# Kernel optimization log

Measured on AMD Instinct MI355X. Metric: run time of the kernel, lower is better.

## Reference

```python
import jax, jax.numpy as jnp
import numpy as np

EPS = 1e-8  # matches torch cosine_similarity eps


def setup_inputs() -> dict:
    key = jax.random.key(0)
    ks = jax.random.split(key, 8)
    B, D_IN, H, L = 256, 256, 256, 100000
    G = 5 * H  # (N_GATES + 1) * hidden_dim
    s_in = 1.0 / np.sqrt(D_IN)
    s_h = 1.0 / np.sqrt(H)
    return {
        "x_t": jax.random.normal(ks[0], (B, D_IN), jnp.float32),
        "h": jax.random.normal(ks[1], (B, H), jnp.float32),
        "c": jax.random.normal(ks[2], (B, H), jnp.float32),
        "W_i2h": jax.random.normal(ks[3], (G, D_IN), jnp.float32) * s_in,
        "b_i2h": jnp.zeros((G,), jnp.float32),
        "W_h2h": jax.random.normal(ks[4], (G, H), jnp.float32) * s_h,
        "b_h2h": jnp.zeros((G,), jnp.float32),
        "keys": jax.random.normal(ks[5], (L, D_IN), jnp.float32),
        "vals": jax.random.normal(ks[6], (L, H), jnp.float32),
    }


def _dnd_get_memory(q, keys, vals):
    # cosine similarity of each query against every stored key -> [B, L]
    qn = q / jnp.maximum(jnp.linalg.norm(q, axis=-1, keepdims=True), EPS)
    kn = keys / jnp.maximum(jnp.linalg.norm(keys, axis=-1, keepdims=True), EPS)
    sims = jnp.einsum("bd,ld->bl", qn, kn)
    w = jax.nn.softmax(sims, axis=-1)          # softmax-weighted aggregation
    return jnp.einsum("bl,lh->bh", w, vals)    # [B, H]


def reference(x_t, h, c, W_i2h, b_i2h, W_h2h, b_h2h, keys, vals):
    H = h.shape[1]
    preact = (x_t @ W_i2h.T + b_i2h) + (h @ W_h2h.T + b_h2h)   # [B, 5H]
    gates = jax.nn.sigmoid(preact[:, : 4 * H])
    f_t = gates[:, :H]
    i_t = gates[:, H:2 * H]
    o_t = gates[:, 2 * H:3 * H]
    r_t = gates[:, 3 * H:4 * H]
    c_t_new = jnp.tanh(preact[:, 4 * H:])
    c_t = f_t * c + i_t * c_t_new
    m_t = jnp.tanh(_dnd_get_memory(x_t, keys, vals))
    c_t = c_t + r_t * m_t
    h_t = o_t * jnp.tanh(c_t)
    return (h_t, c_t)
```

## Files before the change

### kernel.cpp

```cpp
#include <hip/hip_runtime.h>
#include <stdint.h>

typedef float f4_t __attribute__((ext_vector_type(4)));
typedef __bf16 bf8_t __attribute__((ext_vector_type(8)));
typedef unsigned short us4_t __attribute__((ext_vector_type(4)));
typedef unsigned short us8_t __attribute__((ext_vector_type(8)));

static __device__ __forceinline__ unsigned short fbf(float f) {
    __bf16 b = (__bf16)f;
    return *(unsigned short*)&b;
}
static __device__ __forceinline__ float bf2f(unsigned short u) {
    union { uint32_t u; float f; } v; v.u = ((uint32_t)u) << 16;
    return v.f;
}
static __device__ __forceinline__ f4_t mfma16(bf8_t a, bf8_t b, f4_t c) {
    return __builtin_amdgcn_mfma_f32_16x16x32_bf16(a, b, c, 0, 0, 0);
}
static __device__ __forceinline__ float sigf(float x) {
    return 1.0f / (1.0f + __expf(-x));
}
static __device__ __forceinline__ void gload_lds16(const void* g, void* l) {
    __builtin_amdgcn_global_load_lds(
        (const __attribute__((address_space(1))) void*)g,
        (__attribute__((address_space(3))) void*)l, 16, 0, 0);
}

__global__ __launch_bounds__(256) void k_convert(
    const float* __restrict__ x, const float* __restrict__ h,
    const float* __restrict__ W1, const float* __restrict__ W2,
    unsigned short* __restrict__ qn, unsigned short* __restrict__ xb,
    unsigned short* __restrict__ hb, unsigned short* __restrict__ w1b,
    unsigned short* __restrict__ w2b)
{
    __shared__ float sred[4];
    int bid = blockIdx.x, t = threadIdx.x;
    if (bid < 256) {
        float v = x[bid * 256 + t];
        float ss = v * v;
        #pragma unroll
        for (int m = 1; m < 64; m <<= 1) ss += __shfl_xor(ss, m, 64);
        if ((t & 63) == 0) sred[t >> 6] = ss;
        __syncthreads();
        float tot = sred[0] + sred[1] + sred[2] + sred[3];
        float rn = 1.0f / fmaxf(sqrtf(tot), 1e-8f);
        xb[bid * 256 + t] = fbf(v);
        qn[bid * 256 + t] = fbf(v * rn);
    } else if (bid < 512) {
        int b = bid - 256;
        hb[b * 256 + t] = fbf(h[b * 256 + t]);
    } else {
        int i0 = (bid - 512) * 256 + t;
        for (int i = i0; i < 1280 * 256; i += 512 * 256) {
            w1b[i] = fbf(W1[i]);
            w2b[i] = fbf(W2[i]);
        }
    }
}

__global__ __launch_bounds__(256) void k_gates(
    const unsigned short* __restrict__ xb, const unsigned short* __restrict__ hb,
    const unsigned short* __restrict__ w1b, const unsigned short* __restrict__ w2b,
    const float* __restrict__ b1, const float* __restrict__ b2,
    float* __restrict__ pre)
{
    int bb = (blockIdx.x & 3) * 64;
    int gb = (blockIdx.x >> 2) * 64;
    int t = threadIdx.x, w = t >> 6, lane = t & 63;
    int l15 = lane & 15, q8 = (lane >> 4) * 8, q4 = (lane >> 4) * 4;
    int arow = bb + w * 16 + l15;

    f4_t acc[4] = {};
    #pragma unroll
    for (int ks = 0; ks < 8; ++ks) {
        bf8_t a = *(const bf8_t*)&xb[arow * 256 + ks * 32 + q8];
        #pragma unroll
        for (int gc = 0; gc < 4; ++gc) {
            bf8_t bf = *(const bf8_t*)&w1b[(gb + gc * 16 + l15) * 256 + ks * 32 + q8];
            acc[gc] = mfma16(a, bf, acc[gc]);
        }
    }
    #pragma unroll
    for (int ks = 0; ks < 8; ++ks) {
        bf8_t a = *(const bf8_t*)&hb[arow * 256 + ks * 32 + q8];
        #pragma unroll
        for (int gc = 0; gc < 4; ++gc) {
            bf8_t bf = *(const bf8_t*)&w2b[(gb + gc * 16 + l15) * 256 + ks * 32 + q8];
            acc[gc] = mfma16(a, bf, acc[gc]);
        }
    }
    #pragma unroll
    for (int gc = 0; gc < 4; ++gc) {
        int g = gb + gc * 16 + l15;
        float bias = b1[g] + b2[g];
        #pragma unroll
        for (int r = 0; r < 4; ++r) {
            int b = bb + w * 16 + q4 + r;
            pre[b * 1280 + g] = acc[gc][r] + bias;
        }
    }
}

__global__ __launch_bounds__(512, 2) void k_dnd(
    const float* __restrict__ keys, const float* __restrict__ vals,
    const unsigned short* __restrict__ qn,
    unsigned short* __restrict__ opart, float* __restrict__ dpart,
    int L, int CH)
{
    __shared__ __align__(16) char smem[114688];
    unsigned short* Pl = (unsigned short*)(smem + 98304);

    const int t = threadIdx.x;
    const int w = t >> 6, lane = t & 63;
    const int l15 = lane & 15;
    const int q8 = (lane >> 4) * 8, q4 = (lane >> 4) * 4;

    const int bid = blockIdx.x;
    const int hhalf = (bid >> 3) & 1;
    const int chunk = (bid & 7) | ((bid >> 4) << 3);
    const int base = chunk * CH;
    int nkeys = L - base;
    if (nkeys > CH) nkeys = CH;
    if (nkeys < 0) nkeys = 0;
    const int nt = (nkeys + 31) >> 5;

    bf8_t qa[2][8];
    #pragma unroll
    for (int bt = 0; bt < 2; ++bt)
        #pragma unroll
        for (int ks = 0; ks < 8; ++ks)
            qa[bt][ks] = *(const bf8_t*)&qn[(w * 32 + bt * 16 + l15) * 256 + ks * 32 + q8];

    f4_t o[2][8] = {};
    float den[2][4] = {};

    auto issueRaw = [&](int tt) {
        #pragma unroll
        for (int i = 0; i < 4; ++i) {
            int lrow = 4 * w + i;
            int row = base + tt * 32 + lrow;
            if (row >= L) row = L - 1;
            gload_lds16(keys + (size_t)row * 256 + lane * 4,
                        smem + lrow * 1024);
        }
        #pragma unroll
        for (int c = 0; c < 2; ++c) {
            int lrow = 4 * w + 2 * c;
            int row = base + tt * 32 + lrow + (lane >> 5);
            if (row >= L) row = L - 1;
            gload_lds16(vals + (size_t)row * 256 + hhalf * 128 + (lane & 31) * 4,
                        smem + 32768 + lrow * 512);
        }
    };

    auto convert = [&](int buf) {
        unsigned short* Kb = (unsigned short*)(smem + 49152 + buf * 16384);
        unsigned short* Vb = (unsigned short*)(smem + 81920 + buf * 8192);
        const float* Kraw = (const float*)smem;
        const float* Vraw = (const float*)(smem + 32768);
        {
            int row = t >> 4, c16 = (t & 15) * 16;
            f4_t a0 = *(const f4_t*)&Kraw[row * 256 + c16];
            f4_t a1 = *(const f4_t*)&Kraw[row * 256 + c16 + 4];
            f4_t a2 = *(const f4_t*)&Kraw[row * 256 + c16 + 8];
            f4_t a3 = *(const f4_t*)&Kraw[row * 256 + c16 + 12];
            float ss = a0[0]*a0[0]+a0[1]*a0[1]+a0[2]*a0[2]+a0[3]*a0[3]
                     + a1[0]*a1[0]+a1[1]*a1[1]+a1[2]*a1[2]+a1[3]*a1[3]
                     + a2[0]*a2[0]+a2[1]*a2[1]+a2[2]*a2[2]+a2[3]*a2[3]
                     + a3[0]*a3[0]+a3[1]*a3[1]+a3[2]*a3[2]+a3[3]*a3[3];
            ss += __shfl_xor(ss, 1, 64);
            ss += __shfl_xor(ss, 2, 64);
            ss += __shfl_xor(ss, 4, 64);
            ss += __shfl_xor(ss, 8, 64);
            float rn = 1.0f / fmaxf(sqrtf(ss), 1e-8f);
            int sw = (row & 7) * 8;
            us8_t u0, u1;
            u0[0]=fbf(a0[0]*rn); u0[1]=fbf(a0[1]*rn); u0[2]=fbf(a0[2]*rn); u0[3]=fbf(a0[3]*rn);
            u0[4]=fbf(a1[0]*rn); u0[5]=fbf(a1[1]*rn); u0[6]=fbf(a1[2]*rn); u0[7]=fbf(a1[3]*rn);
            u1[0]=fbf(a2[0]*rn); u1[1]=fbf(a2[1]*rn); u1[2]=fbf(a2[2]*rn); u1[3]=fbf(a2[3]*rn);
            u1[4]=fbf(a3[0]*rn); u1[5]=fbf(a3[1]*rn); u1[6]=fbf(a3[2]*rn); u1[7]=fbf(a3[3]*rn);
            *(us8_t*)&Kb[row * 256 + (c16 ^ sw)]       = u0;
            *(us8_t*)&Kb[row * 256 + ((c16 + 8) ^ sw)] = u1;
        }
        {
            int hh = t & 127, oct = t >> 7;
            us8_t uv;
            #pragma unroll
            for (int r = 0; r < 8; ++r)
                uv[r] = fbf(Vraw[(oct * 8 + r) * 128 + hh]);
            int slot = (((hh & 15) * 4 + oct) ^ ((hh & 14) >> 1));
            *(us8_t*)&Vb[(hh >> 4) * 512 + slot * 8] = uv;
        }
    };

    if (nt > 0) {
        issueRaw(0);
        asm volatile("s_waitcnt vmcnt(0)" ::: "memory");
        __builtin_amdgcn_s_barrier();
        convert(0);
        asm volatile("s_waitcnt lgkmcnt(0)\n\ts_barrier" ::: "memory");
        if (nt > 1) issueRaw(1);

        for (int tt = 0; tt < nt; ++tt) {
            const int cur = tt & 1;
            const unsigned short* Kb = (const unsigned short*)(smem + 49152 + cur * 16384);
            const unsigned short* Vb = (const unsigned short*)(smem + 81920 + cur * 8192);

            f4_t s[2][2] = {};
            __builtin_amdgcn_s_setprio(1);
            #pragma unroll
            for (int lc = 0; lc < 2; ++lc) {
                int l = lc * 16 + l15;
                int sw = (l & 7) * 8;
                #pragma unroll
                for (int ks = 0; ks < 8; ++ks) {
                    bf8_t kf = *(const bf8_t*)&Kb[l * 256 + ((ks * 32 + q8) ^ sw)];
                    s[0][lc] = mfma16(qa[0][ks], kf, s[0][lc]);
                    s[1][lc] = mfma16(qa[1][ks], kf, s[1][lc]);
                }
            }
            __builtin_amdgcn_s_setprio(0);

            #pragma unroll
            for (int lc = 0; lc < 2; ++lc) {
                int l = lc * 16 + l15;
                bool valid = (tt * 32 + l) < nkeys;
                #pragma unroll
                for (int bt = 0; bt < 2; ++bt)
                    #pragma unroll
                    for (int r = 0; r < 4; ++r) {
                        float p = valid ? __expf(s[bt][lc][r] - 1.0f) : 0.0f;
                        den[bt][r] += p;
                        int b = w * 32 + bt * 16 + q4 + r;
                        Pl[b * 32 + l] = fbf(p);
                    }
            }

            {
                bf8_t pa0 = *(const bf8_t*)&Pl[(w * 32 + l15) * 32 + q8];
                bf8_t pa1 = *(const bf8_t*)&Pl[(w * 32 + 16 + l15) * 32 + q8];
                __builtin_amdgcn_s_setprio(1);
                #pragma unroll
                for (int hc = 0; hc < 8; ++hc) {
                    int hh = hc * 16 + l15;
                    int slot = (((hh & 15) * 4 + (q8 >> 3)) ^ ((hh & 14) >> 1));
                    bf8_t vf = *(const bf8_t*)&Vb[hc * 512 + slot * 8];
                    o[0][hc] = mfma16(pa0, vf, o[0][hc]);
                    o[1][hc] = mfma16(pa1, vf, o[1][hc]);
                }
                __builtin_amdgcn_s_setprio(0);
            }

            if (tt + 1 < nt) {
                asm volatile("s_waitcnt vmcnt(0)" ::: "memory");
                __builtin_amdgcn_s_barrier();
                convert(cur ^ 1);
                asm volatile("s_waitcnt lgkmcnt(0)\n\ts_barrier" ::: "memory");
                if (tt + 2 < nt) issueRaw(tt + 2);
            }
        }
    }

    asm volatile("s_waitcnt vmcnt(0)" ::: "memory");
    __syncthreads();
    unsigned short* Ol = (unsigned short*)smem;
    #pragma unroll
    for (int bt = 0; bt < 2; ++bt)
        #pragma unroll
        for (int hc = 0; hc < 8; ++hc)
            #pragma unroll
            for (int r = 0; r < 4; ++r)
                Ol[(w * 32 + bt * 16 + q4 + r) * 128 + hc * 16 + l15] = fbf(o[bt][hc][r]);
    __syncthreads();
    {
        size_t ob = (size_t)(chunk * 2 + hhalf) * 32768;
        #pragma unroll
        for (int it = 0; it < 8; ++it) {
            int off = it * 4096 + t * 8;
            *(us8_t*)&opart[ob + off] = *(const us8_t*)&Ol[off];
        }
    }
    if (hhalf == 0) {
        #pragma unroll
        for (int bt = 0; bt < 2; ++bt)
            #pragma unroll
            for (int r = 0; r < 4; ++r) {
                float d = den[bt][r];
                #pragma unroll
                for (int m = 1; m < 16; m <<= 1) d += __shfl_xor(d, m, 64);
                if (l15 == 0)
                    dpart[chunk * 256 + w * 32 + bt * 16 + q4 + r] = d;
            }
    }
}

__global__ __launch_bounds__(256) void k_reduce(
    const unsigned short* __restrict__ opart, const float* __restrict__ dpart,
    const float* __restrict__ pre, const float* __restrict__ c_in,
    float* __restrict__ out)
{
    __shared__ float sred[4];
    int b = blockIdx.x, t = threadIdx.x;

    float ds = (t < 128) ? dpart[t * 256 + b] : 0.0f;
    #pragma unroll
    for (int m = 1; m < 64; m <<= 1) ds += __shfl_xor(ds, m, 64);
    if ((t & 63) == 0) sred[t >> 6] = ds;
    __syncthreads();
    float dtot = fmaxf(sred[0] + sred[1] + sred[2] + sred[3], 1e-30f);

    int bh = t >> 7, hcol = t & 127;
    size_t sb = (size_t)b * 128 + hcol + (size_t)bh * 32768;
    float n0 = 0.f, n1 = 0.f, n2 = 0.f, n3 = 0.f;
    for (int ck = 0; ck < 128; ck += 4) {
        n0 += bf2f(opart[(size_t)(ck + 0) * 65536 + sb]);
        n1 += bf2f(opart[(size_t)(ck + 1) * 65536 + sb]);
        n2 += bf2f(opart[(size_t)(ck + 2) * 65536 + sb]);
        n3 += bf2f(opart[(size_t)(ck + 3) * 65536 + sb]);
    }
    float num = (n0 + n1) + (n2 + n3);

    float m = tanhf(num / dtot);
    const float* p = pre + b * 1280;
    float fg = sigf(p[t]);
    float ig = sigf(p[256 + t]);
    float og = sigf(p[512 + t]);
    float rg = sigf(p[768 + t]);
    float cn = tanhf(p[1024 + t]);
    float co = c_in[b * 256 + t];
    float ct = fg * co + ig * cn + rg * m;
    float ht = og * tanhf(ct);
    out[b * 256 + t] = ht;
    out[65536 + b * 256 + t] = ct;
}

extern "C" void kernel_launch(void* const* d_in, const int* in_sizes, int n_in,
                              void* d_out, int out_size, void* d_ws, size_t ws_size,
                              hipStream_t stream)
{
    const float* x    = (const float*)d_in[0];
    const float* h    = (const float*)d_in[1];
    const float* c    = (const float*)d_in[2];
    const float* W1   = (const float*)d_in[3];
    const float* b1   = (const float*)d_in[4];
    const float* W2   = (const float*)d_in[5];
    const float* b2   = (const float*)d_in[6];
    const float* keys = (const float*)d_in[7];
    const float* vals = (const float*)d_in[8];
    int L = in_sizes[7] / 256;

    int TILES = (L + 128 * 32 - 1) / (128 * 32);
    int CH = TILES * 32;

    char* ws = (char*)d_ws;
    unsigned short* qn    = (unsigned short*)(ws + 0);
    unsigned short* xb    = (unsigned short*)(ws + 131072);
    unsigned short* hb    = (unsigned short*)(ws + 262144);
    unsigned short* w1b   = (unsigned short*)(ws + 393216);
    unsigned short* w2b   = (unsigned short*)(ws + 1048576);
    float*          pre   = (float*)(ws + 1703936);
    float*          dpart = (float*)(ws + 3014656);
    unsigned short* opart = (unsigned short*)(ws + 3145728);

    k_convert<<<dim3(1024), dim3(256), 0, stream>>>(x, h, W1, W2, qn, xb, hb, w1b, w2b);
    k_gates<<<dim3(80), dim3(256), 0, stream>>>(xb, hb, w1b, w2b, b1, b2, pre);
    k_dnd<<<dim3(256), dim3(512), 0, stream>>>(keys, vals, qn, opart, dpart, L, CH);
    k_reduce<<<dim3(256), dim3(256), 0, stream>>>(opart, dpart, pre, c, (float*)d_out);

    (void)n_in; (void)out_size; (void)ws_size;
}
```

Measured before the change: 99.82 us.

## Halve DND key tile to 16 rows, double grid and raise occupancy

The DND kernel now stages 16 keys per step instead of 32, cutting shared memory from about 112KB to 62KB and asking for 4 waves per SIMD in launch bounds. The grid doubles to 512 blocks (256 chunks × 2 hidden halves), and the P·V MFMA runs every second step across two 16-key halves packed into padded LDS rows. This is meant to improve latency hiding and CU coverage, at the cost of more barriers per key, fewer registers per thread, twice as many partial outputs for the reduce kernel to sum, and a two-pass output write.

```diff
diff --git a/kernel.cpp b/kernel.cpp
--- a/kernel.cpp
+++ b/kernel.cpp
@@ -101,19 +101,19 @@
     }
 }
 
-__global__ __launch_bounds__(512, 2) void k_dnd(
+__global__ __launch_bounds__(512, 4) void k_dnd(
     const float* __restrict__ keys, const float* __restrict__ vals,
     const unsigned short* __restrict__ qn,
     unsigned short* __restrict__ opart, float* __restrict__ dpart,
     int L, int CH)
 {
-    __shared__ __align__(16) char smem[114688];
-    unsigned short* Pl = (unsigned short*)(smem + 98304);
+    __shared__ __align__(16) char smem[63488];
+    unsigned short* Kb = (unsigned short*)(smem + 24576);
 
     const int t = threadIdx.x;
     const int w = t >> 6, lane = t & 63;
     const int l15 = lane & 15;
-    const int q8 = (lane >> 4) * 8, q4 = (lane >> 4) * 4;
+    const int q = lane >> 4, q8 = q * 8, q4 = q * 4;
 
     const int bid = blockIdx.x;
     const int hhalf = (bid >> 3) & 1;
@@ -122,7 +122,8 @@
     int nkeys = L - base;
     if (nkeys > CH) nkeys = CH;
     if (nkeys < 0) nkeys = 0;
-    const int nt = (nkeys + 31) >> 5;
+    const int nt = (nkeys + 15) >> 4;
+    const int nt2 = (nt + 1) & ~1;
 
     bf8_t qa[2][8];
     #pragma unroll
@@ -135,147 +136,123 @@
     float den[2][4] = {};
 
     auto issueRaw = [&](int tt) {
-        #pragma unroll
-        for (int i = 0; i < 4; ++i) {
-            int lrow = 4 * w + i;
-            int row = base + tt * 32 + lrow;
+        int r0 = base + tt * 16;
+        #pragma unroll
+        for (int i = 0; i < 2; ++i) {
+            int row = r0 + 2 * w + i;
             if (row >= L) row = L - 1;
             gload_lds16(keys + (size_t)row * 256 + lane * 4,
-                        smem + lrow * 1024);
-        }
-        #pragma unroll
-        for (int c = 0; c < 2; ++c) {
-            int lrow = 4 * w + 2 * c;
-            int row = base + tt * 32 + lrow + (lane >> 5);
-            if (row >= L) row = L - 1;
-            gload_lds16(vals + (size_t)row * 256 + hhalf * 128 + (lane & 31) * 4,
-                        smem + 32768 + lrow * 512);
-        }
+                        smem + (2 * w + i) * 1024);
+        }
+        int vrow = r0 + 2 * w + (lane >> 5);
+        if (vrow >= L) vrow = L - 1;
+        gload_lds16(vals + (size_t)vrow * 256 + hhalf * 128 + (lane & 31) * 4,
+                    smem + 16384 + w * 1024);
     };
 
-    auto convert = [&](int buf) {
-        unsigned short* Kb = (unsigned short*)(smem + 49152 + buf * 16384);
-        unsigned short* Vb = (unsigned short*)(smem + 81920 + buf * 8192);
+    auto convert = [&](int tt) {
         const float* Kraw = (const float*)smem;
-        const float* Vraw = (const float*)(smem + 32768);
-        {
-            int row = t >> 4, c16 = (t & 15) * 16;
-            f4_t a0 = *(const f4_t*)&Kraw[row * 256 + c16];
-            f4_t a1 = *(const f4_t*)&Kraw[row * 256 + c16 + 4];
-            f4_t a2 = *(const f4_t*)&Kraw[row * 256 + c16 + 8];
-            f4_t a3 = *(const f4_t*)&Kraw[row * 256 + c16 + 12];
-            float ss = a0[0]*a0[0]+a0[1]*a0[1]+a0[2]*a0[2]+a0[3]*a0[3]
-                     + a1[0]*a1[0]+a1[1]*a1[1]+a1[2]*a1[2]+a1[3]*a1[3]
-                     + a2[0]*a2[0]+a2[1]*a2[1]+a2[2]*a2[2]+a2[3]*a2[3]
-                     + a3[0]*a3[0]+a3[1]*a3[1]+a3[2]*a3[2]+a3[3]*a3[3];
-            ss += __shfl_xor(ss, 1, 64);
-            ss += __shfl_xor(ss, 2, 64);
-            ss += __shfl_xor(ss, 4, 64);
-            ss += __shfl_xor(ss, 8, 64);
+        #pragma unroll
+        for (int i = 0; i < 2; ++i) {
+            int r = w + i * 8;
+            f4_t v = *(const f4_t*)&Kraw[r * 256 + lane * 4];
+            float ss = v[0]*v[0] + v[1]*v[1] + v[2]*v[2] + v[3]*v[3];
+            #pragma unroll
+            for (int m = 1; m < 64; m <<= 1) ss += __shfl_xor(ss, m, 64);
             float rn = 1.0f / fmaxf(sqrtf(ss), 1e-8f);
-            int sw = (row & 7) * 8;
-            us8_t u0, u1;
-            u0[0]=fbf(a0[0]*rn); u0[1]=fbf(a0[1]*rn); u0[2]=fbf(a0[2]*rn); u0[3]=fbf(a0[3]*rn);
-            u0[4]=fbf(a1[0]*rn); u0[5]=fbf(a1[1]*rn); u0[6]=fbf(a1[2]*rn); u0[7]=fbf(a1[3]*rn);
-            u1[0]=fbf(a2[0]*rn); u1[1]=fbf(a2[1]*rn); u1[2]=fbf(a2[2]*rn); u1[3]=fbf(a2[3]*rn);
-            u1[4]=fbf(a3[0]*rn); u1[5]=fbf(a3[1]*rn); u1[6]=fbf(a3[2]*rn); u1[7]=fbf(a3[3]*rn);
-            *(us8_t*)&Kb[row * 256 + (c16 ^ sw)]       = u0;
-            *(us8_t*)&Kb[row * 256 + ((c16 + 8) ^ sw)] = u1;
-        }
-        {
-            int hh = t & 127, oct = t >> 7;
-            us8_t uv;
-            #pragma unroll
-            for (int r = 0; r < 8; ++r)
-                uv[r] = fbf(Vraw[(oct * 8 + r) * 128 + hh]);
-            int slot = (((hh & 15) * 4 + oct) ^ ((hh & 14) >> 1));
-            *(us8_t*)&Vb[(hh >> 4) * 512 + slot * 8] = uv;
-        }
+            us4_t uv;
+            uv[0] = fbf(v[0]*rn); uv[1] = fbf(v[1]*rn);
+            uv[2] = fbf(v[2]*rn); uv[3] = fbf(v[3]*rn);
+            *(us4_t*)&Kb[r * 256 + ((lane * 4) ^ ((r & 7) * 8))] = uv;
+        }
+        const float* Vraw = (const float*)(smem + 16384);
+        unsigned short* Vb = (unsigned short*)(smem + 32768);
+        int hh = t & 127, lq = t >> 7;
+        us4_t uv;
+        #pragma unroll
+        for (int j = 0; j < 4; ++j)
+            uv[j] = fbf(Vraw[(lq * 4 + j) * 128 + hh]);
+        *(us4_t*)&Vb[hh * 40 + (tt & 1) * 16 + lq * 4] = uv;
     };
 
-    if (nt > 0) {
+    if (nt2 > 0) {
         issueRaw(0);
         asm volatile("s_waitcnt vmcnt(0)" ::: "memory");
         __builtin_amdgcn_s_barrier();
         convert(0);
         asm volatile("s_waitcnt lgkmcnt(0)\n\ts_barrier" ::: "memory");
-        if (nt > 1) issueRaw(1);
-
-        for (int tt = 0; tt < nt; ++tt) {
-            const int cur = tt & 1;
-            const unsigned short* Kb = (const unsigned short*)(smem + 49152 + cur * 16384);
-            const unsigned short* Vb = (const unsigned short*)(smem + 81920 + cur * 8192);
-
-            f4_t s[2][2] = {};
+        if (nt2 > 1) issueRaw(1);
+
+        for (int tt = 0; tt < nt2; ++tt) {
+            f4_t s[2] = {};
             __builtin_amdgcn_s_setprio(1);
             #pragma unroll
-            for (int lc = 0; lc < 2; ++lc) {
-                int l = lc * 16 + l15;
-                int sw = (l & 7) * 8;
-                #pragma unroll
-                for (int ks = 0; ks < 8; ++ks) {
-                    bf8_t kf = *(const bf8_t*)&Kb[l * 256 + ((ks * 32 + q8) ^ sw)];
-                    s[0][lc] = mfma16(qa[0][ks], kf, s[0][lc]);
-                    s[1][lc] = mfma16(qa[1][ks], kf, s[1][lc]);
-                }
+            for (int ks = 0; ks < 8; ++ks) {
+                bf8_t kf = *(const bf8_t*)&Kb[l15 * 256 + ((ks * 32 + q8) ^ ((l15 & 7) * 8))];
+                s[0] = mfma16(qa[0][ks], kf, s[0]);
+                s[1] = mfma16(qa[1][ks], kf, s[1]);
             }
             __builtin_amdgcn_s_setprio(0);
 
-            #pragma unroll
-            for (int lc = 0; lc < 2; ++lc) {
-                int l = lc * 16 + l15;
-                bool valid = (tt * 32 + l) < nkeys;
+            {
+                unsigned short* P = (unsigned short*)(smem + 43008);
+                bool valid = (tt * 16 + l15) < nkeys;
                 #pragma unroll
                 for (int bt = 0; bt < 2; ++bt)
                     #pragma unroll
                     for (int r = 0; r < 4; ++r) {
-                        float p = valid ? __expf(s[bt][lc][r] - 1.0f) : 0.0f;
+                        float p = valid ? __expf(s[bt][r] - 1.0f) : 0.0f;
                         den[bt][r] += p;
                         int b = w * 32 + bt * 16 + q4 + r;
-                        Pl[b * 32 + l] = fbf(p);
+                        P[b * 40 + (tt & 1) * 16 + l15] = fbf(p);
                     }
             }
 
-            {
-                bf8_t pa0 = *(const bf8_t*)&Pl[(w * 32 + l15) * 32 + q8];
-                bf8_t pa1 = *(const bf8_t*)&Pl[(w * 32 + 16 + l15) * 32 + q8];
+            if (tt & 1) {
+                const unsigned short* P = (const unsigned short*)(smem + 43008);
+                const unsigned short* Vb = (const unsigned short*)(smem + 32768);
+                bf8_t pa0 = *(const bf8_t*)&P[(w * 32 + l15) * 40 + q8];
+                bf8_t pa1 = *(const bf8_t*)&P[(w * 32 + 16 + l15) * 40 + q8];
                 __builtin_amdgcn_s_setprio(1);
                 #pragma unroll
                 for (int hc = 0; hc < 8; ++hc) {
                     int hh = hc * 16 + l15;
-                    int slot = (((hh & 15) * 4 + (q8 >> 3)) ^ ((hh & 14) >> 1));
-                    bf8_t vf = *(const bf8_t*)&Vb[hc * 512 + slot * 8];
+                    bf8_t vf = *(const bf8_t*)&Vb[hh * 40 + q8];
                     o[0][hc] = mfma16(pa0, vf, o[0][hc]);
                     o[1][hc] = mfma16(pa1, vf, o[1][hc]);
                 }
                 __builtin_amdgcn_s_setprio(0);
             }
 
-            if (tt + 1 < nt) {
+            if (tt + 1 < nt2) {
                 asm volatile("s_waitcnt vmcnt(0)" ::: "memory");
                 __builtin_amdgcn_s_barrier();
-                convert(cur ^ 1);
+                convert(tt + 1);
                 asm volatile("s_waitcnt lgkmcnt(0)\n\ts_barrier" ::: "memory");
-                if (tt + 2 < nt) issueRaw(tt + 2);
+                if (tt + 2 < nt2) issueRaw(tt + 2);
             }
         }
     }
 
     asm volatile("s_waitcnt vmcnt(0)" ::: "memory");
-    __syncthreads();
     unsigned short* Ol = (unsigned short*)smem;
     #pragma unroll
-    for (int bt = 0; bt < 2; ++bt)
-        #pragma unroll
-        for (int hc = 0; hc < 8; ++hc)
+    for (int p = 0; p < 2; ++p) {
+        __syncthreads();
+        if ((w >> 2) == p) {
+            int wl = w & 3;
             #pragma unroll
-            for (int r = 0; r < 4; ++r)
-                Ol[(w * 32 + bt * 16 + q4 + r) * 128 + hc * 16 + l15] = fbf(o[bt][hc][r]);
-    __syncthreads();
-    {
-        size_t ob = (size_t)(chunk * 2 + hhalf) * 32768;
-        #pragma unroll
-        for (int it = 0; it < 8; ++it) {
+            for (int bt = 0; bt < 2; ++bt)
+                #pragma unroll
+                for (int hc = 0; hc < 8; ++hc)
+                    #pragma unroll
+                    for (int r = 0; r < 4; ++r)
+                        Ol[(wl * 32 + bt * 16 + q4 + r) * 128 + hc * 16 + l15] = fbf(o[bt][hc][r]);
+        }
+        __syncthreads();
+        size_t ob = (size_t)(chunk * 2 + hhalf) * 32768 + (size_t)p * 16384;
+        #pragma unroll
+        for (int it = 0; it < 4; ++it) {
             int off = it * 4096 + t * 8;
             *(us8_t*)&opart[ob + off] = *(const us8_t*)&Ol[off];
         }
@@ -302,7 +279,7 @@
     __shared__ float sred[4];
     int b = blockIdx.x, t = threadIdx.x;
 
-    float ds = (t < 128) ? dpart[t * 256 + b] : 0.0f;
+    float ds = dpart[t * 256 + b];
     #pragma unroll
     for (int m = 1; m < 64; m <<= 1) ds += __shfl_xor(ds, m, 64);
     if ((t & 63) == 0) sred[t >> 6] = ds;
@@ -312,7 +289,7 @@
     int bh = t >> 7, hcol = t & 127;
     size_t sb = (size_t)b * 128 + hcol + (size_t)bh * 32768;
     float n0 = 0.f, n1 = 0.f, n2 = 0.f, n3 = 0.f;
-    for (int ck = 0; ck < 128; ck += 4) {
+    for (int ck = 0; ck < 256; ck += 4) {
         n0 += bf2f(opart[(size_t)(ck + 0) * 65536 + sb]);
         n1 += bf2f(opart[(size_t)(ck + 1) * 65536 + sb]);
         n2 += bf2f(opart[(size_t)(ck + 2) * 65536 + sb]);
@@ -349,8 +326,8 @@
     const float* vals = (const float*)d_in[8];
     int L = in_sizes[7] / 256;
 
-    int TILES = (L + 128 * 32 - 1) / (128 * 32);
-    int CH = TILES * 32;
+    int TILES = (L + 256 * 16 - 1) / (256 * 16);
+    int CH = TILES * 16;
 
     char* ws = (char*)d_ws;
     unsigned short* qn    = (unsigned short*)(ws + 0);
@@ -360,11 +337,11 @@
     unsigned short* w2b   = (unsigned short*)(ws + 1048576);
     float*          pre   = (float*)(ws + 1703936);
     float*          dpart = (float*)(ws + 3014656);
-    unsigned short* opart = (unsigned short*)(ws + 3145728);
+    unsigned short* opart = (unsigned short*)(ws + 3276800);
 
     k_convert<<<dim3(1024), dim3(256), 0, stream>>>(x, h, W1, W2, qn, xb, hb, w1b, w2b);
     k_gates<<<dim3(80), dim3(256), 0, stream>>>(xb, hb, w1b, w2b, b1, b2, pre);
-    k_dnd<<<dim3(256), dim3(512), 0, stream>>>(keys, vals, qn, opart, dpart, L, CH);
+    k_dnd<<<dim3(512), dim3(512), 0, stream>>>(keys, vals, qn, opart, dpart, L, CH);
     k_reduce<<<dim3(256), dim3(256), 0, stream>>>(opart, dpart, pre, c, (float*)d_out);
 
     (void)n_in; (void)out_size; (void)ws_size;
```

Result: slower. 332.1 us (+232.8%).
